# Optimization experiments

Measured on AMD Instinct MI355X. Metric: run time of the kernel, lower is better.

The kernel has to match this reference:

```python
import jax, jax.numpy as jnp
import numpy as np

# Module hyperparameters (see init_kwargs)
P1, P2 = 32, 32      # num_patches_h, num_patches_w (256/8)
H1, W2 = 8, 8        # patch_size
CH = 3               # input channels
CI, SI = 768, 4      # num_cores, rfs_per_capsule (capsule_size=256, rf_size=64)
KOUT, LOUT = 256, 4  # output_cores, slots per output core
PROBA = 0.1          # connection_proba


def setup_inputs() -> dict:
    key = jax.random.key(0)
    kx, kc = jax.random.split(key)
    x = jax.random.normal(kx, (128, 256, 256, 3), dtype=jnp.float32)
    # fast_scrramble: fixed random-sparse binary connectivity tensor
    # [source_core, source_slot, dest_core, dest_slot]
    C = jax.random.bernoulli(kc, PROBA, (CI, SI, KOUT, LOUT)).astype(jnp.float32)
    return {"x": x, "C": C}


def reference(x, C):
    b = x.shape[0]
    # 'b (p1 h1) (p2 w2) c -> b p1 p2 h1 w2 c'
    x = x.reshape(b, P1, H1, P2, W2, CH).transpose(0, 1, 3, 2, 4, 5)
    # 'b p1 p2 h1 w2 c -> b h1 w2 (p1 p2 c)'
    x = x.transpose(0, 3, 4, 1, 2, 5).reshape(b, H1, W2, P1 * P2 * CH)
    # 'b h1 w2 (ci si) -> b ci si h1 w2'
    x = x.reshape(b, H1, W2, CI, SI).transpose(0, 3, 4, 1, 2)
    # Literal einsum from the source: no shared labels between operands,
    # so this is sum_{c,s} x (per b,h,w) times sum_{i,j} C (per k,l).
    return jnp.einsum('bcshw,ijkl->bklhw', x, C)
```

## Files before the change

kernel.cpp:

```cpp
#include <hip/hip_runtime.h>


__global__ __launch_bounds__(256) void reduce_C_kernel(const float* __restrict__ C,
                                                       float* __restrict__ sC) {
    const int col  = blockIdx.x * 256 + threadIdx.x;
    const int row0 = blockIdx.y * 32;
    const float* p = C + (size_t)row0 * 1024 + col;
    float s = 0.f;
#pragma unroll
    for (int r = 0; r < 32; ++r) s += p[r * 1024];
    atomicAdd(sC + col, s);
}

__global__ __launch_bounds__(192) void reduce_x_kernel(const float* __restrict__ x,
                                                       float* __restrict__ sx) {
    const int b  = blockIdx.y;
    const int y0 = blockIdx.x * 32;
    const int t  = threadIdx.x;
    const float* base = x + ((size_t)b * 256 + y0) * 768;

    float acc[8];
#pragma unroll
    for (int h = 0; h < 8; ++h) acc[h] = 0.f;

#pragma unroll
    for (int h = 0; h < 8; ++h) {
#pragma unroll
        for (int j = 0; j < 4; ++j) {
            const float* rowp = base + (size_t)(h + 8 * j) * 768;
#pragma unroll
            for (int it = 0; it < 4; ++it)
                acc[h] += rowp[it * 192 + t];
        }
    }

    __shared__ float lds[192][8];
#pragma unroll
    for (int h = 0; h < 8; ++h) lds[t][h] = acc[h];
    __syncthreads();

    if (t < 64) {
        const int h = t >> 3, w = t & 7;
        float s = 0.f;
#pragma unroll
        for (int g = 0; g < 8; ++g)
#pragma unroll
            for (int c = 0; c < 3; ++c)
                s += lds[g * 24 + w * 3 + c][h];
        atomicAdd(sx + b * 64 + t, s);
    }
}

__global__ __launch_bounds__(256) void expand_kernel(const float* __restrict__ sx,
                                                     const float* __restrict__ sC,
                                                     float4* __restrict__ out) {
    const int b   = blockIdx.y;
    const int idx = blockIdx.x * 256 + threadIdx.x;
    const int hw4 = idx & 15;
    const int kl  = idx >> 4;
    const float4 v = ((const float4*)(sx + b * 64))[hw4];
    const float  s = sC[kl];
    float4 r;
    r.x = v.x * s; r.y = v.y * s; r.z = v.z * s; r.w = v.w * s;
    out[(size_t)b * 16384 + idx] = r;
}

extern "C" void kernel_launch(void* const* d_in, const int* in_sizes, int n_in,
                              void* d_out, int out_size, void* d_ws, size_t ws_size,
                              hipStream_t stream) {
    const float* x = (const float*)d_in[0];
    const float* C = (const float*)d_in[1];
    float* out = (float*)d_out;

    float* sC = (float*)d_ws;
    float* sx = (float*)d_ws + 1024;

    hipMemsetAsync(d_ws, 0, (1024 + 8192) * sizeof(float), stream);

    reduce_C_kernel<<<dim3(4, 96),  256, 0, stream>>>(C, sC);
    reduce_x_kernel<<<dim3(8, 128), 192, 0, stream>>>(x, sx);
    expand_kernel<<<dim3(64, 128),  256, 0, stream>>>(sx, sC, (float4*)out);
}
```

Baseline: 171.8 us.

## Replace atomics and memset with two-stage partial reductions and vectorized loads

Drops the workspace memset and the atomicAdd accumulation. C and x are now reduced into per-block partial sums, read with float4 loads, and the final C column sums are folded into the x-reduction kernel (only blocks with b==0 do this work). The expand kernel sums the x partials once per block into shared memory and writes four float4 outputs per thread. This removes one launch and the atomic contention, at the cost of extra workspace traffic and a serialized 96-deep sum done by a few blocks.

After: 189.2 us. 10.1% more time.

```diff
diff --git a/kernel.cpp b/kernel.cpp
--- a/kernel.cpp
+++ b/kernel.cpp
@@ -1,68 +1,98 @@
 #include <hip/hip_runtime.h>
 
 
-__global__ __launch_bounds__(256) void reduce_C_kernel(const float* __restrict__ C,
-                                                       float* __restrict__ sC) {
-    const int col  = blockIdx.x * 256 + threadIdx.x;
-    const int row0 = blockIdx.y * 32;
-    const float* p = C + (size_t)row0 * 1024 + col;
-    float s = 0.f;
+#define PSX_ELEMS (128 * 8 * 64)
+#define PSC_ELEMS (96 * 1024)
+
+__global__ __launch_bounds__(256) void reduce_C_part(const float* __restrict__ C,
+                                                     float4* __restrict__ psC) {
+    const int p = blockIdx.x;
+    const int t = threadIdx.x;
+    const float4* row = (const float4*)(C + (size_t)p * 32 * 1024) + t;
+    float4 a = {0.f, 0.f, 0.f, 0.f};
 #pragma unroll
-    for (int r = 0; r < 32; ++r) s += p[r * 1024];
-    atomicAdd(sC + col, s);
+    for (int r = 0; r < 32; ++r) {
+        float4 v = row[(size_t)r * 256];
+        a.x += v.x; a.y += v.y; a.z += v.z; a.w += v.w;
+    }
+    psC[p * 256 + t] = a;
 }
 
-__global__ __launch_bounds__(192) void reduce_x_kernel(const float* __restrict__ x,
-                                                       float* __restrict__ sx) {
+__global__ __launch_bounds__(384) void reduce_x_part(const float* __restrict__ x,
+                                                     const float* __restrict__ psC,
+                                                     float* __restrict__ psx,
+                                                     float* __restrict__ sC) {
     const int b  = blockIdx.y;
-    const int y0 = blockIdx.x * 32;
+    const int bx = blockIdx.x;
     const int t  = threadIdx.x;
-    const float* base = x + ((size_t)b * 256 + y0) * 768;
+    const float4* base4 = (const float4*)(x + ((size_t)b * 256 + bx * 32) * 768);
 
-    float acc[8];
+    float4 acc[4];
 #pragma unroll
-    for (int h = 0; h < 8; ++h) acc[h] = 0.f;
+    for (int mm = 0; mm < 4; ++mm) acc[mm] = (float4){0.f, 0.f, 0.f, 0.f};
 
 #pragma unroll
-    for (int h = 0; h < 8; ++h) {
+    for (int jj = 0; jj < 4; ++jj)
 #pragma unroll
-        for (int j = 0; j < 4; ++j) {
-            const float* rowp = base + (size_t)(h + 8 * j) * 768;
+        for (int mm = 0; mm < 4; ++mm) {
+            float4 v = base4[(size_t)(mm + 4 * jj) * 384 + t];
+            acc[mm].x += v.x; acc[mm].y += v.y; acc[mm].z += v.z; acc[mm].w += v.w;
+        }
+
+    __shared__ float4 lds4[8][193];
+    const int r  = t / 192;
+    const int c4 = t % 192;
 #pragma unroll
-            for (int it = 0; it < 4; ++it)
-                acc[h] += rowp[it * 192 + t];
-        }
-    }
-
-    __shared__ float lds[192][8];
-#pragma unroll
-    for (int h = 0; h < 8; ++h) lds[t][h] = acc[h];
+    for (int mm = 0; mm < 4; ++mm) lds4[2 * mm + r][c4] = acc[mm];
     __syncthreads();
 
     if (t < 64) {
         const int h = t >> 3, w = t & 7;
+        const float* L = (const float*)&lds4[h][0];
         float s = 0.f;
 #pragma unroll
-        for (int g = 0; g < 8; ++g)
+        for (int g = 0; g < 32; ++g)
+            s += L[3 * w + 24 * g] + L[3 * w + 1 + 24 * g] + L[3 * w + 2 + 24 * g];
+        psx[(size_t)b * 512 + bx * 64 + t] = s;
+    }
+
+    if (b == 0 && t < 128) {
+        const int col = bx * 128 + t;
+        float s = 0.f;
 #pragma unroll
-            for (int c = 0; c < 3; ++c)
-                s += lds[g * 24 + w * 3 + c][h];
-        atomicAdd(sx + b * 64 + t, s);
+        for (int p = 0; p < 96; ++p) s += psC[p * 1024 + col];
+        sC[col] = s;
     }
 }
 
-__global__ __launch_bounds__(256) void expand_kernel(const float* __restrict__ sx,
+__global__ __launch_bounds__(256) void expand_kernel(const float* __restrict__ psx,
                                                      const float* __restrict__ sC,
                                                      float4* __restrict__ out) {
-    const int b   = blockIdx.y;
-    const int idx = blockIdx.x * 256 + threadIdx.x;
-    const int hw4 = idx & 15;
-    const int kl  = idx >> 4;
-    const float4 v = ((const float4*)(sx + b * 64))[hw4];
-    const float  s = sC[kl];
-    float4 r;
-    r.x = v.x * s; r.y = v.y * s; r.z = v.z * s; r.w = v.w * s;
-    out[(size_t)b * 16384 + idx] = r;
+    const int b  = blockIdx.y;
+    const int bx = blockIdx.x;
+    const int t  = threadIdx.x;
+
+    __shared__ float4 sxl4[16];
+    __shared__ float  sCl[64];
+
+    if (t < 64) {
+        float s = 0.f;
+#pragma unroll
+        for (int g = 0; g < 8; ++g) s += psx[(size_t)b * 512 + g * 64 + t];
+        ((float*)sxl4)[t] = s;
+    } else if (t < 128) {
+        sCl[t - 64] = sC[bx * 64 + (t - 64)];
+    }
+    __syncthreads();
+
+    const float4 v = sxl4[t & 15];
+    float4* ob = out + (size_t)b * 16384 + bx * 1024 + t;
+#pragma unroll
+    for (int u = 0; u < 4; ++u) {
+        const float s = sCl[(t >> 4) + 16 * u];
+        float4 rr; rr.x = v.x * s; rr.y = v.y * s; rr.z = v.z * s; rr.w = v.w * s;
+        ob[256 * u] = rr;
+    }
 }
 
 extern "C" void kernel_launch(void* const* d_in, const int* in_sizes, int n_in,
@@ -72,12 +102,11 @@
     const float* C = (const float*)d_in[1];
     float* out = (float*)d_out;
 
-    float* sC = (float*)d_ws;
-    float* sx = (float*)d_ws + 1024;
+    float* psx = (float*)d_ws;
+    float* psC = psx + PSX_ELEMS;
+    float* sC  = psC + PSC_ELEMS;
 
-    hipMemsetAsync(d_ws, 0, (1024 + 8192) * sizeof(float), stream);
-
-    reduce_C_kernel<<<dim3(4, 96),  256, 0, stream>>>(C, sC);
-    reduce_x_kernel<<<dim3(8, 128), 192, 0, stream>>>(x, sx);
-    expand_kernel<<<dim3(64, 128),  256, 0, stream>>>(sx, sC, (float4*)out);
+    reduce_C_part<<<dim3(96), 256, 0, stream>>>(C, (float4*)psC);
+    reduce_x_part<<<dim3(8, 128), 384, 0, stream>>>(x, psC, psx, sC);
+    expand_kernel<<<dim3(16, 128), 256, 0, stream>>>(psx, sC, (float4*)out);
 }
```
